# Kernel optimization log

Hardware: AMD Instinct MI355X
Metric: run time of the kernel (lower is better)

## Reference

```python
import jax, jax.numpy as jnp
import numpy as np

N_DIM = 1024   # nodes (rows of s, rows of Kweight)
IN_DIM = 1024  # nodes / feature dim (cols of s, rows of Qweight, side of Gmat)
H_DIM = 64
B = 16


def setup_inputs() -> dict:
    key = jax.random.key(0)
    k1, k2, k3, k4 = jax.random.split(key, 4)
    s = jax.random.normal(k1, (N_DIM, B, IN_DIM), dtype=jnp.float32)
    Gmat = jax.random.uniform(k2, (IN_DIM, IN_DIM), dtype=jnp.float32)
    # torch init: rand * (4/d)**0.5 - (1/d)**0.5  => U[-(1/d)**0.5, (1/d)**0.5]... kept faithful
    Qweight = jax.random.uniform(k3, (IN_DIM, H_DIM), dtype=jnp.float32) * (4.0 / IN_DIM) ** 0.5 - (1.0 / IN_DIM) ** 0.5
    Kweight = jax.random.uniform(k4, (N_DIM, H_DIM), dtype=jnp.float32) * (4.0 / N_DIM) ** 0.5 - (1.0 / N_DIM) ** 0.5
    return {"s": s, "Gmat": Gmat, "Qweight": Qweight, "Kweight": Kweight}


def reference(s, Gmat, Qweight, Kweight):
    h_dim = Qweight.shape[1]
    inv_sqrt_h = 1.0 / jnp.sqrt(jnp.float32(h_dim))
    # q: einsum('ijk,km->ijm', s, Qw).permute(1,0,2) -> (B, n, h)
    q = jnp.einsum('nbi,ih->bnh', s, Qweight)
    # k: s.permute(1,2,0) einsum Kw then permute(0,2,1) -> (B, h, i)
    k = jnp.einsum('nbi,nh->bhi', s, Kweight)
    # squared (non-softmax) attention scores: (B, n, i)
    att = jnp.square(jnp.einsum('bnh,bhi->bni', q, k) * inv_sqrt_h + 1e-9)
    # adjacency aggregation: (B, n, i) @ (i, i)
    att = jnp.einsum('bni,ij->bnj', att, Gmat)
    # row-normalize and permute back to (n, B, i)
    s_t = jnp.sum(att, axis=2, keepdims=True) + 0.001
    return (att / s_t).transpose(1, 0, 2)
```

## Files before the change

### kernel.cpp

```cpp
#include <hip/hip_runtime.h>
#include <hip/hip_bf16.h>
#include <stdint.h>

typedef unsigned short u16;
typedef unsigned int   u32;

#define N_DIM  1024
#define IN_DIM 1024
#define H_DIM  64
#define BATCH  16

typedef __bf16 bf16x8 __attribute__((ext_vector_type(8)));
typedef float  f32x4  __attribute__((ext_vector_type(4)));

__device__ inline u16 f2bf(float f) {
    union { float f; u32 u; } v; v.f = f;
    u32 u = v.u;
    u32 r = (u + 0x7fffu + ((u >> 16) & 1u)) >> 16;
    return (u16)r;
}
__device__ inline float bf2f(u32 bits16) {
    union { u32 u; float f; } v; v.u = bits16 << 16;
    return v.f;
}

__device__ inline void gl_lds16(const u16* g, u16* l) {
    __builtin_amdgcn_global_load_lds(
        (const __attribute__((address_space(1))) u32*)g,
        (__attribute__((address_space(3))) u32*)l, 16, 0, 0);
}

__global__ void prep_w(const float* __restrict__ Q, const float* __restrict__ Kw,
                       u16* __restrict__ QT, u16* __restrict__ KwT) {
    int idx = blockIdx.x * 256 + threadIdx.x;
    const float* src = (idx < 65536) ? Q : Kw;
    u16* dst = (idx < 65536) ? QT : KwT;
    int i = idx & 65535;
    int h = i >> 10;
    int n = i & 1023;
    dst[h * 1024 + n] = f2bf(src[n * 64 + h]);
}

__global__ void prep_g(const float* __restrict__ G, u16* __restrict__ Gbt,
                       float* __restrict__ Grsum) {
    __shared__ float tile[64][65];
    int i0 = blockIdx.y * 64, j0 = blockIdx.x * 64;
    int tx = threadIdx.x & 63, ty = threadIdx.x >> 6;
    for (int r = 0; r < 16; ++r) {
        int i = ty * 16 + r;
        tile[i][tx] = G[(size_t)(i0 + i) * 1024 + j0 + tx];
    }
    __syncthreads();
    for (int r = 0; r < 16; ++r) {
        int j = ty * 16 + r;
        Gbt[(size_t)(j0 + j) * 1024 + i0 + tx] = f2bf(tile[tx][j]);
    }
    if (ty == 0) {
        float sum = 0.f;
        for (int j = 0; j < 64; ++j) sum += tile[tx][j];
        atomicAdd(&Grsum[i0 + tx], sum);
    }
}

__global__ void prep_s(const float* __restrict__ s, u16* __restrict__ sb,
                       u16* __restrict__ sbT) {
    __shared__ u16 tile[64][65];
    int b = blockIdx.z, n0 = blockIdx.y * 64, i0 = blockIdx.x * 64;
    int tx = threadIdx.x & 63, ty = threadIdx.x >> 6;
    for (int r = 0; r < 16; ++r) {
        int n = ty * 16 + r;
        size_t gi = (size_t)(n0 + n) * (BATCH * IN_DIM) + (size_t)b * IN_DIM + i0 + tx;
        u16 bv = f2bf(s[gi]);
        sb[gi] = bv;
        tile[n][tx] = bv;
    }
    __syncthreads();
    for (int r = 0; r < 16; ++r) {
        int i = ty * 16 + r;
        sbT[(size_t)b * (IN_DIM * N_DIM) + (size_t)(i0 + i) * N_DIM + n0 + tx] = tile[tx][i];
    }
}

__global__ __launch_bounds__(256) void gemm_qkt(
        const u16* __restrict__ sb, const u16* __restrict__ sbT,
        const u16* __restrict__ QT, const u16* __restrict__ KwT,
        u16* __restrict__ qws, u16* __restrict__ ktws) {
    int z = blockIdx.z, b = z & 15;
    const u16* A; size_t ldA; const u16* Bt; u16* out;
    if (z < 16) { A = sb  + (size_t)b * IN_DIM;          ldA = BATCH * IN_DIM; Bt = QT;  out = qws  + (size_t)b * (N_DIM * H_DIM); }
    else        { A = sbT + (size_t)b * (IN_DIM * N_DIM); ldA = N_DIM;         Bt = KwT; out = ktws + (size_t)b * (IN_DIM * H_DIM); }
    int m0 = blockIdx.x * 128;
    __shared__ u16 As[128 * 32];
    __shared__ u16 Bs[64 * 32];
    int t = threadIdx.x, lane = t & 63, w = t >> 6;
    f32x4 acc[2][4] = {};
    for (int k0 = 0; k0 < 1024; k0 += 32) {
        int r = t >> 2, c = (t & 3) * 8;
        gl_lds16(A + (size_t)(m0 + r) * ldA + k0 + c,      &As[r * 32 + c]);
        gl_lds16(A + (size_t)(m0 + r + 64) * ldA + k0 + c, &As[(r + 64) * 32 + c]);
        gl_lds16(Bt + (size_t)r * 1024 + k0 + c,           &Bs[r * 32 + c]);
        __syncthreads();
        int kh = (lane >> 4) * 8;
        bf16x8 af[2], bfr[4];
        for (int rt = 0; rt < 2; ++rt)
            af[rt] = *(const bf16x8*)&As[(w * 32 + rt * 16 + (lane & 15)) * 32 + kh];
        for (int ct = 0; ct < 4; ++ct)
            bfr[ct] = *(const bf16x8*)&Bs[(ct * 16 + (lane & 15)) * 32 + kh];
        for (int rt = 0; rt < 2; ++rt)
            for (int ct = 0; ct < 4; ++ct)
                acc[rt][ct] = __builtin_amdgcn_mfma_f32_16x16x32_bf16(af[rt], bfr[ct], acc[rt][ct], 0, 0, 0);
        __syncthreads();
    }
    for (int rt = 0; rt < 2; ++rt)
        for (int ct = 0; ct < 4; ++ct)
            for (int r = 0; r < 4; ++r) {
                int m = w * 32 + rt * 16 + (lane >> 4) * 4 + r;
                int n = ct * 16 + (lane & 15);
                out[(size_t)(m0 + m) * H_DIM + n] = f2bf(acc[rt][ct][r]);
            }
}

__global__ __launch_bounds__(256) void gemm_score(
        const u16* __restrict__ qws, const u16* __restrict__ ktws,
        u16* __restrict__ att) {
    int b = blockIdx.z;
    const u16* A  = qws  + (size_t)b * (N_DIM * H_DIM);
    const u16* Bt = ktws + (size_t)b * (IN_DIM * H_DIM);
    int m0 = blockIdx.y * 128, n0 = blockIdx.x * 128;
    __shared__ u16 As[128 * 32];
    __shared__ u16 Bs[128 * 32];
    int t = threadIdx.x, lane = t & 63, w = t >> 6;
    int wm = (w >> 1) * 64, wn = (w & 1) * 64;
    f32x4 acc[4][4] = {};
    for (int k0 = 0; k0 < 64; k0 += 32) {
        int r = t >> 2, c = (t & 3) * 8;
        gl_lds16(A  + (size_t)(m0 + r) * 64 + k0 + c,      &As[r * 32 + c]);
        gl_lds16(A  + (size_t)(m0 + r + 64) * 64 + k0 + c, &As[(r + 64) * 32 + c]);
        gl_lds16(Bt + (size_t)(n0 + r) * 64 + k0 + c,      &Bs[r * 32 + c]);
        gl_lds16(Bt + (size_t)(n0 + r + 64) * 64 + k0 + c, &Bs[(r + 64) * 32 + c]);
        __syncthreads();
        int kh = (lane >> 4) * 8;
        bf16x8 af[4], bfr[4];
        for (int i = 0; i < 4; ++i)
            af[i] = *(const bf16x8*)&As[(wm + i * 16 + (lane & 15)) * 32 + kh];
        for (int j = 0; j < 4; ++j)
            bfr[j] = *(const bf16x8*)&Bs[(wn + j * 16 + (lane & 15)) * 32 + kh];
        for (int i = 0; i < 4; ++i)
            for (int j = 0; j < 4; ++j)
                acc[i][j] = __builtin_amdgcn_mfma_f32_16x16x32_bf16(af[i], bfr[j], acc[i][j], 0, 0, 0);
        __syncthreads();
    }
    for (int i = 0; i < 4; ++i)
        for (int j = 0; j < 4; ++j)
            for (int r = 0; r < 4; ++r) {
                int m = m0 + wm + i * 16 + (lane >> 4) * 4 + r;
                int n = n0 + wn + j * 16 + (lane & 15);
                float v = acc[i][j][r] * 0.125f + 1e-9f;
                v = v * v;
                att[(size_t)b * (N_DIM * IN_DIM) + (size_t)m * IN_DIM + n] = f2bf(v);
            }
}

__global__ void rowsum_k(const u16* __restrict__ att, const float* __restrict__ Grsum,
                         float* __restrict__ rinv) {
    int bn = blockIdx.x;
    const u16* row = att + (size_t)bn * 1024;
    int t = threadIdx.x;
    uint2 p = ((const uint2*)row)[t];
    float4 g = ((const float4*)Grsum)[t];
    float sum = bf2f(p.x & 0xffffu) * g.x + bf2f(p.x >> 16) * g.y
              + bf2f(p.y & 0xffffu) * g.z + bf2f(p.y >> 16) * g.w;
    for (int off = 32; off; off >>= 1) sum += __shfl_down(sum, off, 64);
    __shared__ float ws[4];
    if ((t & 63) == 0) ws[t >> 6] = sum;
    __syncthreads();
    if (t == 0) rinv[bn] = 1.0f / (ws[0] + ws[1] + ws[2] + ws[3] + 0.001f);
}

__global__ __launch_bounds__(256) void gemm_big(
        const u16* __restrict__ att, const u16* __restrict__ Gbt,
        const float* __restrict__ rinv, float* __restrict__ out) {
    int b = blockIdx.z;
    const u16* A = att + (size_t)b * (N_DIM * IN_DIM);
    int m0 = blockIdx.y * 128, n0 = blockIdx.x * 128;
    __shared__ u16 As[128 * 32];
    __shared__ u16 Bs[128 * 32];
    int t = threadIdx.x, lane = t & 63, w = t >> 6;
    int wm = (w >> 1) * 64, wn = (w & 1) * 64;
    f32x4 acc[4][4] = {};
    for (int k0 = 0; k0 < 1024; k0 += 32) {
        int r = t >> 2, c = (t & 3) * 8;
        gl_lds16(A   + (size_t)(m0 + r) * 1024 + k0 + c,      &As[r * 32 + c]);
        gl_lds16(A   + (size_t)(m0 + r + 64) * 1024 + k0 + c, &As[(r + 64) * 32 + c]);
        gl_lds16(Gbt + (size_t)(n0 + r) * 1024 + k0 + c,      &Bs[r * 32 + c]);
        gl_lds16(Gbt + (size_t)(n0 + r + 64) * 1024 + k0 + c, &Bs[(r + 64) * 32 + c]);
        __syncthreads();
        int kh = (lane >> 4) * 8;
        bf16x8 af[4], bfr[4];
        for (int i = 0; i < 4; ++i)
            af[i] = *(const bf16x8*)&As[(wm + i * 16 + (lane & 15)) * 32 + kh];
        for (int j = 0; j < 4; ++j)
            bfr[j] = *(const bf16x8*)&Bs[(wn + j * 16 + (lane & 15)) * 32 + kh];
        for (int i = 0; i < 4; ++i)
            for (int j = 0; j < 4; ++j)
                acc[i][j] = __builtin_amdgcn_mfma_f32_16x16x32_bf16(af[i], bfr[j], acc[i][j], 0, 0, 0);
        __syncthreads();
    }
    for (int i = 0; i < 4; ++i)
        for (int r = 0; r < 4; ++r) {
            int m = m0 + wm + i * 16 + (lane >> 4) * 4 + r;
            float rv = rinv[b * 1024 + m];
            for (int j = 0; j < 4; ++j) {
                int n = n0 + wn + j * 16 + (lane & 15);
                out[(size_t)m * (BATCH * IN_DIM) + (size_t)b * IN_DIM + n] = acc[i][j][r] * rv;
            }
        }
}

extern "C" void kernel_launch(void* const* d_in, const int* in_sizes, int n_in,
                              void* d_out, int out_size, void* d_ws, size_t ws_size,
                              hipStream_t stream) {
    const float* s  = (const float*)d_in[0];
    const float* G  = (const float*)d_in[1];
    const float* Q  = (const float*)d_in[2];
    const float* Kw = (const float*)d_in[3];
    float* out = (float*)d_out;
    char* ws = (char*)d_ws;

    u16*  sb    = (u16*)(ws);
    u16*  sbT   = (u16*)(ws + (size_t)(32u << 20));
    u16*  qws   = (u16*)(ws + (size_t)(64u << 20));
    u16*  ktws  = (u16*)(ws + (size_t)(66u << 20));
    u16*  Gbt   = (u16*)(ws + (size_t)(68u << 20));
    u16*  QT    = (u16*)(ws + (size_t)(70u << 20));
    u16*  KwT   = (u16*)(ws + (size_t)(70u << 20) + (128u << 10));
    float* Grsum= (float*)(ws + (size_t)(70u << 20) + (256u << 10));
    float* rinv = (float*)(ws + (size_t)(70u << 20) + (260u << 10));
    u16*  att   = sb;

    hipMemsetAsync(Grsum, 0, 1024 * sizeof(float), stream);
    prep_w<<<512, 256, 0, stream>>>(Q, Kw, QT, KwT);
    prep_g<<<dim3(16, 16), 256, 0, stream>>>(G, Gbt, Grsum);
    prep_s<<<dim3(16, 16, 16), 256, 0, stream>>>(s, sb, sbT);
    gemm_qkt<<<dim3(8, 1, 32), 256, 0, stream>>>(sb, sbT, QT, KwT, qws, ktws);
    gemm_score<<<dim3(8, 8, 16), 256, 0, stream>>>(qws, ktws, att);
    rowsum_k<<<16384, 256, 0, stream>>>(att, Grsum, rinv);
    gemm_big<<<dim3(8, 8, 16), 256, 0, stream>>>(att, Gbt, rinv, out);
}
```

Baseline: 238.5 us.

## Fuse score, rowsum and G-aggregation GEMMs; read fp32 s directly in projection

Removes the prep_s conversion/transpose pass and the materialized bf16 attention matrix. gemm_qkt now loads fp32 s directly, converts it to bf16 in registers, and transposes it through LDS for the K path. A single fused kernel recomputes each 128x32 score tile on the fly from q and k, squares it, and accumulates row sums against the G row sums. It then feeds the tile through LDS into the G GEMM with double-buffered G loads and applies the normalization in the epilogue. This avoids large global round trips of the attention matrix, but the score tile is recomputed once per column block (8 times) and the loop carries extra syncs.

```diff
diff --git a/kernel.cpp b/kernel.cpp
--- a/kernel.cpp
+++ b/kernel.cpp
@@ -1,5 +1,4 @@
 #include <hip/hip_runtime.h>
-#include <hip/hip_bf16.h>
 #include <stdint.h>
 
 typedef unsigned short u16;
@@ -16,12 +15,10 @@
 __device__ inline u16 f2bf(float f) {
     union { float f; u32 u; } v; v.f = f;
     u32 u = v.u;
-    u32 r = (u + 0x7fffu + ((u >> 16) & 1u)) >> 16;
-    return (u16)r;
-}
-__device__ inline float bf2f(u32 bits16) {
-    union { u32 u; float f; } v; v.u = bits16 << 16;
-    return v.f;
+    return (u16)((u + 0x7fffu + ((u >> 16) & 1u)) >> 16);
+}
+__device__ inline u32 pack2(float a, float b) {
+    return (u32)f2bf(a) | ((u32)f2bf(b) << 16);
 }
 
 __device__ inline void gl_lds16(const u16* g, u16* l) {
@@ -62,50 +59,50 @@
     }
 }
 
-__global__ void prep_s(const float* __restrict__ s, u16* __restrict__ sb,
-                       u16* __restrict__ sbT) {
-    __shared__ u16 tile[64][65];
-    int b = blockIdx.z, n0 = blockIdx.y * 64, i0 = blockIdx.x * 64;
-    int tx = threadIdx.x & 63, ty = threadIdx.x >> 6;
-    for (int r = 0; r < 16; ++r) {
-        int n = ty * 16 + r;
-        size_t gi = (size_t)(n0 + n) * (BATCH * IN_DIM) + (size_t)b * IN_DIM + i0 + tx;
-        u16 bv = f2bf(s[gi]);
-        sb[gi] = bv;
-        tile[n][tx] = bv;
-    }
-    __syncthreads();
-    for (int r = 0; r < 16; ++r) {
-        int i = ty * 16 + r;
-        sbT[(size_t)b * (IN_DIM * N_DIM) + (size_t)(i0 + i) * N_DIM + n0 + tx] = tile[tx][i];
-    }
-}
-
 __global__ __launch_bounds__(256) void gemm_qkt(
-        const u16* __restrict__ sb, const u16* __restrict__ sbT,
-        const u16* __restrict__ QT, const u16* __restrict__ KwT,
-        u16* __restrict__ qws, u16* __restrict__ ktws) {
-    int z = blockIdx.z, b = z & 15;
-    const u16* A; size_t ldA; const u16* Bt; u16* out;
-    if (z < 16) { A = sb  + (size_t)b * IN_DIM;          ldA = BATCH * IN_DIM; Bt = QT;  out = qws  + (size_t)b * (N_DIM * H_DIM); }
-    else        { A = sbT + (size_t)b * (IN_DIM * N_DIM); ldA = N_DIM;         Bt = KwT; out = ktws + (size_t)b * (IN_DIM * H_DIM); }
+        const float* __restrict__ s, const u16* __restrict__ QT,
+        const u16* __restrict__ KwT, u16* __restrict__ qws, u16* __restrict__ ktws) {
+    int z = blockIdx.z; int b = z & 15; bool isq = (z < 16);
     int m0 = blockIdx.x * 128;
-    __shared__ u16 As[128 * 32];
-    __shared__ u16 Bs[64 * 32];
-    int t = threadIdx.x, lane = t & 63, w = t >> 6;
+    __shared__ __align__(16) u16 As[128 * 40];
+    __shared__ __align__(16) u16 Bs[64 * 40];
+    const u16* Bt = isq ? QT : KwT;
+    u16* outp = (isq ? qws : ktws) + (size_t)b * 65536;
+    int t = threadIdx.x, lane = t & 63, w = t >> 6, quad = lane >> 4, l15 = lane & 15;
     f32x4 acc[2][4] = {};
     for (int k0 = 0; k0 < 1024; k0 += 32) {
-        int r = t >> 2, c = (t & 3) * 8;
-        gl_lds16(A + (size_t)(m0 + r) * ldA + k0 + c,      &As[r * 32 + c]);
-        gl_lds16(A + (size_t)(m0 + r + 64) * ldA + k0 + c, &As[(r + 64) * 32 + c]);
-        gl_lds16(Bt + (size_t)r * 1024 + k0 + c,           &Bs[r * 32 + c]);
-        __syncthreads();
-        int kh = (lane >> 4) * 8;
+        {
+            int h = t >> 2, c = (t & 3) * 8;
+            uint4 v = *(const uint4*)&Bt[(size_t)h * 1024 + k0 + c];
+            *(uint4*)&Bs[h * 40 + c] = v;
+        }
+        if (isq) {
+            int r = t >> 1, c = (t & 1) * 16;
+            const float* src = s + (size_t)(m0 + r) * (BATCH * IN_DIM) + (size_t)b * IN_DIM + k0 + c;
+            float4 f0 = ((const float4*)src)[0];
+            float4 f1 = ((const float4*)src)[1];
+            float4 f2 = ((const float4*)src)[2];
+            float4 f3 = ((const float4*)src)[3];
+            uint4 w0 = { pack2(f0.x,f0.y), pack2(f0.z,f0.w), pack2(f1.x,f1.y), pack2(f1.z,f1.w) };
+            uint4 w1 = { pack2(f2.x,f2.y), pack2(f2.z,f2.w), pack2(f3.x,f3.y), pack2(f3.z,f3.w) };
+            *(uint4*)&As[r * 40 + c]     = w0;
+            *(uint4*)&As[r * 40 + c + 8] = w1;
+        } else {
+            int nr = t >> 3, icb = (t & 7) * 4;
+            const float* src = s + (size_t)(k0 + nr) * (BATCH * IN_DIM) + (size_t)b * IN_DIM + m0;
+            for (int j3 = 0; j3 < 4; ++j3) {
+                float4 f = *(const float4*)&src[icb + 32 * j3];
+                As[(icb + 32*j3 + 0) * 40 + nr] = f2bf(f.x);
+                As[(icb + 32*j3 + 1) * 40 + nr] = f2bf(f.y);
+                As[(icb + 32*j3 + 2) * 40 + nr] = f2bf(f.z);
+                As[(icb + 32*j3 + 3) * 40 + nr] = f2bf(f.w);
+            }
+        }
+        __syncthreads();
+        int kh = quad * 8;
         bf16x8 af[2], bfr[4];
-        for (int rt = 0; rt < 2; ++rt)
-            af[rt] = *(const bf16x8*)&As[(w * 32 + rt * 16 + (lane & 15)) * 32 + kh];
-        for (int ct = 0; ct < 4; ++ct)
-            bfr[ct] = *(const bf16x8*)&Bs[(ct * 16 + (lane & 15)) * 32 + kh];
+        for (int rt = 0; rt < 2; ++rt) af[rt] = *(const bf16x8*)&As[(w*32 + rt*16 + l15) * 40 + kh];
+        for (int ct = 0; ct < 4; ++ct) bfr[ct] = *(const bf16x8*)&Bs[(ct*16 + l15) * 40 + kh];
         for (int rt = 0; rt < 2; ++rt)
             for (int ct = 0; ct < 4; ++ct)
                 acc[rt][ct] = __builtin_amdgcn_mfma_f32_16x16x32_bf16(af[rt], bfr[ct], acc[rt][ct], 0, 0, 0);
@@ -114,107 +111,102 @@
     for (int rt = 0; rt < 2; ++rt)
         for (int ct = 0; ct < 4; ++ct)
             for (int r = 0; r < 4; ++r) {
-                int m = w * 32 + rt * 16 + (lane >> 4) * 4 + r;
-                int n = ct * 16 + (lane & 15);
-                out[(size_t)(m0 + m) * H_DIM + n] = f2bf(acc[rt][ct][r]);
+                int m = w * 32 + rt * 16 + quad * 4 + r;
+                int n = ct * 16 + l15;
+                outp[(size_t)(m0 + m) * 64 + n] = f2bf(acc[rt][ct][r]);
             }
 }
 
-__global__ __launch_bounds__(256) void gemm_score(
+__global__ __launch_bounds__(256) void gemm_fused(
         const u16* __restrict__ qws, const u16* __restrict__ ktws,
-        u16* __restrict__ att) {
+        const u16* __restrict__ Gbt, const float* __restrict__ Grsum,
+        float* __restrict__ out) {
     int b = blockIdx.z;
-    const u16* A  = qws  + (size_t)b * (N_DIM * H_DIM);
-    const u16* Bt = ktws + (size_t)b * (IN_DIM * H_DIM);
-    int m0 = blockIdx.y * 128, n0 = blockIdx.x * 128;
-    __shared__ u16 As[128 * 32];
-    __shared__ u16 Bs[128 * 32];
-    int t = threadIdx.x, lane = t & 63, w = t >> 6;
+    int n0 = blockIdx.x * 128, m0 = blockIdx.y * 128;
+    const u16* qb = qws  + (size_t)b * 65536;
+    const u16* kb = ktws + (size_t)b * 65536;
+    __shared__ __align__(16) u16 As[128 * 40];
+    __shared__ __align__(16) u16 Bs[2][128 * 32];
+    __shared__ __align__(16) u16 ktc[2][32 * 72];
+    __shared__ __align__(16) float Grs[1024];
+    __shared__ float rs[128];
+    int t = threadIdx.x, lane = t & 63, w = t >> 6, quad = lane >> 4, l15 = lane & 15;
+    int ti = w & 1;
     int wm = (w >> 1) * 64, wn = (w & 1) * 64;
+
+    ((float4*)Grs)[t] = ((const float4*)Grsum)[t];
+    if (t < 128) rs[t] = 0.f;
+
+    bf16x8 qf[4][2];
+    for (int j = 0; j < 4; ++j)
+        for (int kick = 0; kick < 2; ++kick)
+            qf[j][kick] = *(const bf16x8*)&qb[(size_t)(m0 + wm + j*16 + l15) * 64 + kick*32 + quad*8];
+
+    int br = t >> 2, bc = (t & 3) * 8;
+    gl_lds16(Gbt + (size_t)(n0 + br) * 1024 + bc,      &Bs[0][br * 32 + bc]);
+    gl_lds16(Gbt + (size_t)(n0 + br + 64) * 1024 + bc, &Bs[0][(br + 64) * 32 + bc]);
+    int ir = t >> 3, ch = (t & 7) * 8;
+    uint4 kreg = *(const uint4*)&kb[(size_t)ir * 64 + ch];
+
     f32x4 acc[4][4] = {};
-    for (int k0 = 0; k0 < 64; k0 += 32) {
-        int r = t >> 2, c = (t & 3) * 8;
-        gl_lds16(A  + (size_t)(m0 + r) * 64 + k0 + c,      &As[r * 32 + c]);
-        gl_lds16(A  + (size_t)(m0 + r + 64) * 64 + k0 + c, &As[(r + 64) * 32 + c]);
-        gl_lds16(Bt + (size_t)(n0 + r) * 64 + k0 + c,      &Bs[r * 32 + c]);
-        gl_lds16(Bt + (size_t)(n0 + r + 64) * 64 + k0 + c, &Bs[(r + 64) * 32 + c]);
-        __syncthreads();
-        int kh = (lane >> 4) * 8;
+    float partial[4] = {0.f, 0.f, 0.f, 0.f};
+
+    for (int kk = 0; kk < 32; ++kk) {
+        int buf = kk & 1;
+        *(uint4*)&ktc[buf][ir * 72 + ch] = kreg;
+        __syncthreads();
+        f32x4 sacc[4] = {};
+        for (int kick = 0; kick < 2; ++kick) {
+            bf16x8 ktf = *(const bf16x8*)&ktc[buf][(ti*16 + l15) * 72 + kick*32 + quad*8];
+            for (int j = 0; j < 4; ++j)
+                sacc[j] = __builtin_amdgcn_mfma_f32_16x16x32_bf16(ktf, qf[j][kick], sacc[j], 0, 0, 0);
+        }
+        if (kk < 31)
+            kreg = *(const uint4*)&kb[(size_t)((kk + 1) * 32 + ir) * 64 + ch];
+        float4 g = *(const float4*)&Grs[kk * 32 + ti * 16 + quad * 4];
+        for (int j = 0; j < 4; ++j) {
+            float v0 = sacc[j][0] * 0.125f + 1e-9f; v0 *= v0;
+            float v1 = sacc[j][1] * 0.125f + 1e-9f; v1 *= v1;
+            float v2 = sacc[j][2] * 0.125f + 1e-9f; v2 *= v2;
+            float v3 = sacc[j][3] * 0.125f + 1e-9f; v3 *= v3;
+            partial[j] += v0 * g.x + v1 * g.y + v2 * g.z + v3 * g.w;
+            uint2 pk = { pack2(v0, v1), pack2(v2, v3) };
+            *(uint2*)&As[(wm + j*16 + l15) * 40 + ti*16 + quad*4] = pk;
+        }
+        __syncthreads();
+        if (kk < 31) {
+            gl_lds16(Gbt + (size_t)(n0 + br) * 1024 + (kk+1)*32 + bc,      &Bs[buf^1][br * 32 + bc]);
+            gl_lds16(Gbt + (size_t)(n0 + br + 64) * 1024 + (kk+1)*32 + bc, &Bs[buf^1][(br + 64) * 32 + bc]);
+        }
+        int kh = quad * 8;
         bf16x8 af[4], bfr[4];
-        for (int i = 0; i < 4; ++i)
-            af[i] = *(const bf16x8*)&As[(wm + i * 16 + (lane & 15)) * 32 + kh];
-        for (int j = 0; j < 4; ++j)
-            bfr[j] = *(const bf16x8*)&Bs[(wn + j * 16 + (lane & 15)) * 32 + kh];
+        for (int i = 0; i < 4; ++i) af[i]  = *(const bf16x8*)&As[(wm + i*16 + l15) * 40 + kh];
+        for (int j = 0; j < 4; ++j) bfr[j] = *(const bf16x8*)&Bs[buf][(wn + j*16 + l15) * 32 + kh];
         for (int i = 0; i < 4; ++i)
             for (int j = 0; j < 4; ++j)
                 acc[i][j] = __builtin_amdgcn_mfma_f32_16x16x32_bf16(af[i], bfr[j], acc[i][j], 0, 0, 0);
-        __syncthreads();
-    }
-    for (int i = 0; i < 4; ++i)
-        for (int j = 0; j < 4; ++j)
-            for (int r = 0; r < 4; ++r) {
-                int m = m0 + wm + i * 16 + (lane >> 4) * 4 + r;
-                int n = n0 + wn + j * 16 + (lane & 15);
-                float v = acc[i][j][r] * 0.125f + 1e-9f;
-                v = v * v;
-                att[(size_t)b * (N_DIM * IN_DIM) + (size_t)m * IN_DIM + n] = f2bf(v);
-            }
-}
-
-__global__ void rowsum_k(const u16* __restrict__ att, const float* __restrict__ Grsum,
-                         float* __restrict__ rinv) {
-    int bn = blockIdx.x;
-    const u16* row = att + (size_t)bn * 1024;
-    int t = threadIdx.x;
-    uint2 p = ((const uint2*)row)[t];
-    float4 g = ((const float4*)Grsum)[t];
-    float sum = bf2f(p.x & 0xffffu) * g.x + bf2f(p.x >> 16) * g.y
-              + bf2f(p.y & 0xffffu) * g.z + bf2f(p.y >> 16) * g.w;
-    for (int off = 32; off; off >>= 1) sum += __shfl_down(sum, off, 64);
-    __shared__ float ws[4];
-    if ((t & 63) == 0) ws[t >> 6] = sum;
+    }
+
+    for (int j = 0; j < 4; ++j) {
+        partial[j] += __shfl_xor(partial[j], 16, 64);
+        partial[j] += __shfl_xor(partial[j], 32, 64);
+    }
+    if (quad == 0)
+        for (int j = 0; j < 4; ++j) atomicAdd(&rs[wm + j*16 + l15], partial[j]);
     __syncthreads();
-    if (t == 0) rinv[bn] = 1.0f / (ws[0] + ws[1] + ws[2] + ws[3] + 0.001f);
-}
-
-__global__ __launch_bounds__(256) void gemm_big(
-        const u16* __restrict__ att, const u16* __restrict__ Gbt,
-        const float* __restrict__ rinv, float* __restrict__ out) {
-    int b = blockIdx.z;
-    const u16* A = att + (size_t)b * (N_DIM * IN_DIM);
-    int m0 = blockIdx.y * 128, n0 = blockIdx.x * 128;
-    __shared__ u16 As[128 * 32];
-    __shared__ u16 Bs[128 * 32];
-    int t = threadIdx.x, lane = t & 63, w = t >> 6;
-    int wm = (w >> 1) * 64, wn = (w & 1) * 64;
-    f32x4 acc[4][4] = {};
-    for (int k0 = 0; k0 < 1024; k0 += 32) {
-        int r = t >> 2, c = (t & 3) * 8;
-        gl_lds16(A   + (size_t)(m0 + r) * 1024 + k0 + c,      &As[r * 32 + c]);
-        gl_lds16(A   + (size_t)(m0 + r + 64) * 1024 + k0 + c, &As[(r + 64) * 32 + c]);
-        gl_lds16(Gbt + (size_t)(n0 + r) * 1024 + k0 + c,      &Bs[r * 32 + c]);
-        gl_lds16(Gbt + (size_t)(n0 + r + 64) * 1024 + k0 + c, &Bs[(r + 64) * 32 + c]);
-        __syncthreads();
-        int kh = (lane >> 4) * 8;
-        bf16x8 af[4], bfr[4];
-        for (int i = 0; i < 4; ++i)
-            af[i] = *(const bf16x8*)&As[(wm + i * 16 + (lane & 15)) * 32 + kh];
-        for (int j = 0; j < 4; ++j)
-            bfr[j] = *(const bf16x8*)&Bs[(wn + j * 16 + (lane & 15)) * 32 + kh];
-        for (int i = 0; i < 4; ++i)
+    if (t < 128) rs[t] = 1.0f / (rs[t] + 0.001f);
+    __syncthreads();
+
+    for (int i = 0; i < 4; ++i) {
+        float4 rv = *(const float4*)&rs[wm + i * 16 + quad * 4];
+        float rva[4] = { rv.x, rv.y, rv.z, rv.w };
+        for (int r = 0; r < 4; ++r) {
+            int m = m0 + wm + i * 16 + quad * 4 + r;
+            float* orow = out + (size_t)m * (BATCH * IN_DIM) + (size_t)b * IN_DIM + n0;
             for (int j = 0; j < 4; ++j)
-                acc[i][j] = __builtin_amdgcn_mfma_f32_16x16x32_bf16(af[i], bfr[j], acc[i][j], 0, 0, 0);
-        __syncthreads();
-    }
-    for (int i = 0; i < 4; ++i)
-        for (int r = 0; r < 4; ++r) {
-            int m = m0 + wm + i * 16 + (lane >> 4) * 4 + r;
-            float rv = rinv[b * 1024 + m];
-            for (int j = 0; j < 4; ++j) {
-                int n = n0 + wn + j * 16 + (lane & 15);
-                out[(size_t)m * (BATCH * IN_DIM) + (size_t)b * IN_DIM + n] = acc[i][j][r] * rv;
-            }
-        }
+                orow[wn + j * 16 + l15] = acc[i][j][r] * rva[r];
+        }
+    }
 }
 
 extern "C" void kernel_launch(void* const* d_in, const int* in_sizes, int n_in,
@@ -227,23 +219,16 @@
     float* out = (float*)d_out;
     char* ws = (char*)d_ws;
 
-    u16*  sb    = (u16*)(ws);
-    u16*  sbT   = (u16*)(ws + (size_t)(32u << 20));
-    u16*  qws   = (u16*)(ws + (size_t)(64u << 20));
-    u16*  ktws  = (u16*)(ws + (size_t)(66u << 20));
-    u16*  Gbt   = (u16*)(ws + (size_t)(68u << 20));
-    u16*  QT    = (u16*)(ws + (size_t)(70u << 20));
-    u16*  KwT   = (u16*)(ws + (size_t)(70u << 20) + (128u << 10));
-    float* Grsum= (float*)(ws + (size_t)(70u << 20) + (256u << 10));
-    float* rinv = (float*)(ws + (size_t)(70u << 20) + (260u << 10));
-    u16*  att   = sb;
+    u16*   qws   = (u16*)(ws);
+    u16*   ktws  = (u16*)(ws + (size_t)(2u << 20));
+    u16*   Gbt   = (u16*)(ws + (size_t)(4u << 20));
+    u16*   QT    = (u16*)(ws + (size_t)(6u << 20));
+    u16*   KwT   = (u16*)(ws + (size_t)(6u << 20) + (128u << 10));
+    float* Grsum = (float*)(ws + (size_t)(6u << 20) + (256u << 10));
 
     hipMemsetAsync(Grsum, 0, 1024 * sizeof(float), stream);
     prep_w<<<512, 256, 0, stream>>>(Q, Kw, QT, KwT);
     prep_g<<<dim3(16, 16), 256, 0, stream>>>(G, Gbt, Grsum);
-    prep_s<<<dim3(16, 16, 16), 256, 0, stream>>>(s, sb, sbT);
-    gemm_qkt<<<dim3(8, 1, 32), 256, 0, stream>>>(sb, sbT, QT, KwT, qws, ktws);
-    gemm_score<<<dim3(8, 8, 16), 256, 0, stream>>>(qws, ktws, att);
-    rowsum_k<<<16384, 256, 0, stream>>>(att, Grsum, rinv);
-    gemm_big<<<dim3(8, 8, 16), 256, 0, stream>>>(att, Gbt, rinv, out);
-}
+    gemm_qkt<<<dim3(8, 1, 32), 256, 0, stream>>>(s, QT, KwT, qws, ktws);
+    gemm_fused<<<dim3(8, 8, 16), 256, 0, stream>>>(qws, ktws, Gbt, Grsum, out);
+}
```

Result: faster. 230.0 us (-3.6%).
